# Kernel optimization log

Measured on AMD Instinct MI355X. Metric: run time of the kernel, lower is better.

## Reference

```python
import jax, jax.numpy as jnp
import numpy as np

B, T, S, L = 1, 2048, 512, 1024
C, H, Hk, D = 2048, 16, 4, 128
THETA = 10000.0


def setup_inputs() -> dict:
    key = jax.random.key(0)
    ks = jax.random.split(key, 9)
    sd = 0.02
    return {
        "x": jax.random.normal(ks[0], (B, T, C), jnp.float32),
        "stm": jax.random.normal(ks[1], (B, S, C), jnp.float32),
        "long_q": jax.random.normal(ks[2], (B, L, H, D), jnp.float32),
        "long_k": jax.random.normal(ks[3], (B, L, Hk, D), jnp.float32),
        "long_v": jax.random.normal(ks[4], (B, L, Hk, D), jnp.float32),
        "Wq": jax.random.normal(ks[5], (C, C), jnp.float32) * sd,
        "Wk": jax.random.normal(ks[6], (C, Hk * D), jnp.float32) * sd,
        "Wv": jax.random.normal(ks[7], (C, Hk * D), jnp.float32) * sd,
        "Wo": jax.random.normal(ks[8], (C, C), jnp.float32) * sd,
    }


def _rope_cos_sin(n, d, theta):
    # precompute_freqs_cis: freqs over even dims, angles t*freq
    freqs = 1.0 / (theta ** (jnp.arange(0, d, 2, dtype=jnp.float32) / d))
    ang = jnp.arange(n, dtype=jnp.float32)[:, None] * freqs[None, :]  # (n, d/2)
    return jnp.cos(ang), jnp.sin(ang)


def _apply_rope(x, cos, sin):
    # x: (B, n, h, D); complex-pair rotation over consecutive dims
    x1, x2 = x[..., 0::2], x[..., 1::2]
    c = cos[None, :, None, :]
    s = sin[None, :, None, :]
    r1 = x1 * c - x2 * s
    r2 = x1 * s + x2 * c
    return jnp.stack([r1, r2], axis=-1).reshape(x.shape)


def reference(x, stm, long_q, long_k, long_v, Wq, Wk, Wv, Wo):
    Bb, Tt, Cc = x.shape
    Ss, Ll = stm.shape[1], long_q.shape[1]
    seq = jnp.concatenate([stm, x], axis=1)  # (B, S+T, C)
    q = jnp.concatenate([long_q, (seq @ Wq).reshape(Bb, Ss + Tt, H, D)], axis=1)
    k = jnp.concatenate([long_k, (seq @ Wk).reshape(Bb, Ss + Tt, Hk, D)], axis=1)
    v = jnp.concatenate([long_v, (seq @ Wv).reshape(Bb, Ss + Tt, Hk, D)], axis=1)
    # inline RoPE on the last T+S positions only (memory bank keeps fixed encoding)
    cos, sin = _rope_cos_sin(Ss + Tt, D, THETA)
    q = q.at[:, Ll:].set(_apply_rope(q[:, Ll:], cos, sin))
    k = k.at[:, Ll:].set(_apply_rope(k[:, Ll:], cos, sin))
    tot = Ll + Ss + Tt
    # structured memory mask: causal over full stream, memory keys (< L+S) visible to all
    idx = jnp.arange(tot)
    mask = (idx[None, :] <= idx[:, None]) | (idx[None, :] < Ll + Ss)  # (tot, tot)
    # GQA: repeat_interleave kv heads
    rep = H // Hk
    kr = jnp.repeat(k, rep, axis=2)  # (B, tot, H, D)
    vr = jnp.repeat(v, rep, axis=2)
    att = jnp.einsum("bihd,bjhd->bhij", q, kr) * (1.0 / np.sqrt(D))
    att = jnp.where(mask[None, None], att, -jnp.inf)
    att = jax.nn.softmax(att, axis=-1)
    y = jnp.einsum("bhij,bjhd->bihd", att, vr).reshape(Bb, tot, Cc)
    y = y[:, -Tt:]  # keep only current-block outputs
    return y @ Wo
```

## Files before the change

### kernel.cpp

```cpp
#include <hip/hip_runtime.h>
#include <hip/hip_bf16.h>

typedef __attribute__((ext_vector_type(8))) short short8;
typedef __attribute__((ext_vector_type(4))) short short4v;
typedef __attribute__((ext_vector_type(4))) float f32x4;
typedef __attribute__((ext_vector_type(4))) float float4v;
typedef __attribute__((ext_vector_type(4))) int i32x4;

#define DEVFN static __device__ __forceinline__

#define T_N   2048
#define S_N   512
#define L_N   1024
#define C_N   2048
#define H_N   16
#define HK_N  4
#define D_N   128
#define ST_N  2560
#define TOT_N 3584
#define KV_N  512

DEVFN short f2bf(float f) {
  union { float f; unsigned u; } v; v.f = f;
  return (short)((v.u + 0x7FFFu + ((v.u >> 16) & 1u)) >> 16);
}
DEVFN float bf2f(short s) {
  union { unsigned u; float f; } v; v.u = ((unsigned)(unsigned short)s) << 16;
  return v.f;
}
DEVFN void gload16(const void* g, void* l) {
  __builtin_amdgcn_global_load_lds(
      (__attribute__((address_space(1))) void*)(g),
      (__attribute__((address_space(3))) void*)(l), 16, 0, 0);
}

#define Q_A (S_N * C_N / 4)
#define Q_B (Q_A + T_N * C_N / 4)
#define Q_C (Q_B + L_N * KV_N / 4)
#define Q_D (Q_C + L_N * KV_N / 4)
#define TAB_E (Q_D + ST_N * 64)
__global__ void k_setup(const float* __restrict__ x, const float* __restrict__ stm,
                        const float* __restrict__ lk, const float* __restrict__ lv,
                        short* __restrict__ seq, short* __restrict__ Kf,
                        short* __restrict__ Vf, float* __restrict__ ct,
                        float* __restrict__ st_) {
  int i = blockIdx.x * 256 + threadIdx.x;
  if (i < Q_D) {
    const float* src; short* dst; int off;
    if (i < Q_A)      { src = stm; dst = seq;                         off = i; }
    else if (i < Q_B) { src = x;   dst = seq + (size_t)S_N * C_N;     off = i - Q_A; }
    else if (i < Q_C) { src = lk;  dst = Kf;                          off = i - Q_B; }
    else              { src = lv;  dst = Vf;                          off = i - Q_C; }
    float4v v = reinterpret_cast<const float4v*>(src)[off];
    short4v o;
    o[0] = f2bf(v[0]); o[1] = f2bf(v[1]); o[2] = f2bf(v[2]); o[3] = f2bf(v[3]);
    reinterpret_cast<short4v*>(dst)[off] = o;
  } else {
    int j = i - Q_D;
    int p = j >> 6, fq = j & 63;
    float freq = expf(-(float)fq * (logf(10000.0f) / 64.0f));
    float ang = (float)p * freq;
    ct[j] = cosf(ang);
    st_[j] = sinf(ang);
  }
}

__global__ void k_tconv_all(const float* __restrict__ Wq, const float* __restrict__ Wk,
                            const float* __restrict__ Wv, const float* __restrict__ Wo,
                            short* __restrict__ WqT, short* __restrict__ WkT,
                            short* __restrict__ WvT, short* __restrict__ WoT) {
  __shared__ float tile[32][33];
  const int z = blockIdx.z;
  const float* in = (z == 0) ? Wq : (z == 1) ? Wk : (z == 2) ? Wv : Wo;
  short* outp     = (z == 0) ? WqT : (z == 1) ? WkT : (z == 2) ? WvT : WoT;
  const int cols = (z == 1 || z == 2) ? KV_N : C_N;
  if (blockIdx.x * 32 >= cols) return;
  int c0 = blockIdx.x * 32, r0 = blockIdx.y * 32;
  int tx = threadIdx.x, ty = threadIdx.y;
#pragma unroll
  for (int i = 0; i < 4; i++)
    tile[ty + i * 8][tx] = in[(size_t)(r0 + ty + i * 8) * cols + c0 + tx];
  __syncthreads();
#pragma unroll
  for (int i = 0; i < 4; i++)
    outp[(size_t)(c0 + ty + i * 8) * C_N + r0 + tx] = f2bf(tile[tx][ty + i * 8]);
}

__global__ void k_tv(const short* __restrict__ vf, short* __restrict__ vt) {
  __shared__ short tile[32][33];
  int hk = blockIdx.z;
  int r0 = blockIdx.x * 32;
  int d0 = blockIdx.y * 32;
  int tx = threadIdx.x, ty = threadIdx.y;
#pragma unroll
  for (int i = 0; i < 4; i++)
    tile[ty + i * 8][tx] = vf[(size_t)(r0 + ty + i * 8) * KV_N + hk * D_N + d0 + tx];
  __syncthreads();
  short* o = vt + (size_t)hk * D_N * TOT_N;
#pragma unroll
  for (int i = 0; i < 4; i++)
    o[(size_t)(d0 + ty + i * 8) * TOT_N + r0 + tx] = tile[tx][ty + i * 8];
}

template <bool OUT_F32>
__global__ __launch_bounds__(256) void k_gemm(
    const short* __restrict__ A, const short* __restrict__ Bt,
    void* __restrict__ C, int M, int N, int K) {
  __shared__ short lbuf[2 * 2 * 4096];
  const int tid = threadIdx.x;
  const int w = tid >> 6, l = tid & 63;
  const int l15 = l & 15, lh = l >> 4;
  const int rb = blockIdx.y << 7, cb = blockIdx.x << 7;
  const int wr = (w >> 1) << 6, wc = (w & 1) << 6;
  f32x4 acc[4][4] = {};
  const int c0 = tid, c1 = 256 + tid;
  const short* pa0 = &A[(size_t)(rb + (c0 >> 2)) * K + (((c0 ^ (c0 >> 2)) & 3) << 3)];
  const short* pa1 = &A[(size_t)(rb + (c1 >> 2)) * K + (((c1 ^ (c1 >> 2)) & 3) << 3)];
  const short* pb0 = &Bt[(size_t)(cb + (c0 >> 2)) * K + (((c0 ^ (c0 >> 2)) & 3) << 3)];
  const short* pb1 = &Bt[(size_t)(cb + (c1 >> 2)) * K + (((c1 ^ (c1 >> 2)) & 3) << 3)];
  const int offA0 = (w * 64) << 4, offA1 = ((256 + w * 64) << 4);
  char* lbase = (char*)lbuf;
  const int sw = (lh ^ (l15 & 3)) << 3;
  {
    gload16(pa0, lbase + offA0);
    gload16(pa1, lbase + offA1);
    gload16(pb0, lbase + 8192 + offA0);
    gload16(pb1, lbase + 8192 + offA1);
  }
  int cur = 0;
  for (int kt = 0; kt < K; kt += 32) {
    const bool more = (kt + 32 < K);
    if (more) {
      char* p = lbase + ((cur ^ 1) << 14);
      gload16(pa0 + kt + 32, p + offA0);
      gload16(pa1 + kt + 32, p + offA1);
      gload16(pb0 + kt + 32, p + 8192 + offA0);
      gload16(pb1 + kt + 32, p + 8192 + offA1);
      asm volatile("s_waitcnt vmcnt(4)" ::: "memory");
    } else {
      asm volatile("s_waitcnt vmcnt(0)" ::: "memory");
    }
    __builtin_amdgcn_s_barrier();
    __builtin_amdgcn_sched_barrier(0);
    const short* la = (const short*)(lbase + (cur << 14));
    const short* lb = (const short*)(lbase + (cur << 14) + 8192);
    short8 af[4], bg[4];
#pragma unroll
    for (int m = 0; m < 4; m++)
      af[m] = *reinterpret_cast<const short8*>(&la[(wr + m * 16 + l15) * 32 + sw]);
#pragma unroll
    for (int n = 0; n < 4; n++)
      bg[n] = *reinterpret_cast<const short8*>(&lb[(wc + n * 16 + l15) * 32 + sw]);
    __builtin_amdgcn_s_setprio(1);
#pragma unroll
    for (int m = 0; m < 4; m++)
#pragma unroll
      for (int n = 0; n < 4; n++)
        acc[m][n] = __builtin_amdgcn_mfma_f32_16x16x32_bf16(af[m], bg[n], acc[m][n], 0, 0, 0);
    __builtin_amdgcn_s_setprio(0);
    asm volatile("s_waitcnt lgkmcnt(0)" ::: "memory");
    __builtin_amdgcn_sched_barrier(0);
    __builtin_amdgcn_s_barrier();
    __builtin_amdgcn_sched_barrier(0);
    cur ^= 1;
  }
#pragma unroll
  for (int m = 0; m < 4; m++)
#pragma unroll
    for (int n = 0; n < 4; n++)
#pragma unroll
      for (int r = 0; r < 4; r++) {
        int row = rb + wr + m * 16 + lh * 4 + r;
        int col = cb + wc + n * 16 + l15;
        if (OUT_F32)
          reinterpret_cast<float*>(C)[(size_t)row * N + col] = acc[m][n][r];
        else
          reinterpret_cast<short*>(C)[(size_t)row * N + col] = f2bf(acc[m][n][r]);
      }
}

__global__ __launch_bounds__(256) void k_gemm_qkv(
    const short* __restrict__ A, const short* __restrict__ Bt,
    short* __restrict__ qbuf, short* __restrict__ Kf, short* __restrict__ Vf,
    const float* __restrict__ ct, const float* __restrict__ st_) {
  const int Kd = C_N;
  __shared__ short lbuf[2 * 2 * 4096];
  const int tid = threadIdx.x;
  const int w = tid >> 6, l = tid & 63;
  const int l15 = l & 15, lh = l >> 4;
  const int rb = blockIdx.y << 7, cb = blockIdx.x << 7;
  const int wr = (w >> 1) << 6, wc = (w & 1) << 6;
  f32x4 acc[4][4] = {};
  const int c0 = tid, c1 = 256 + tid;
  const short* pa0 = &A[(size_t)(rb + (c0 >> 2)) * Kd + (((c0 ^ (c0 >> 2)) & 3) << 3)];
  const short* pa1 = &A[(size_t)(rb + (c1 >> 2)) * Kd + (((c1 ^ (c1 >> 2)) & 3) << 3)];
  const short* pb0 = &Bt[(size_t)(cb + (c0 >> 2)) * Kd + (((c0 ^ (c0 >> 2)) & 3) << 3)];
  const short* pb1 = &Bt[(size_t)(cb + (c1 >> 2)) * Kd + (((c1 ^ (c1 >> 2)) & 3) << 3)];
  const int offA0 = (w * 64) << 4, offA1 = ((256 + w * 64) << 4);
  char* lbase = (char*)lbuf;
  const int sw = (lh ^ (l15 & 3)) << 3;
  {
    gload16(pa0, lbase + offA0);
    gload16(pa1, lbase + offA1);
    gload16(pb0, lbase + 8192 + offA0);
    gload16(pb1, lbase + 8192 + offA1);
  }
  int cur = 0;
  for (int kt = 0; kt < Kd; kt += 32) {
    const bool more = (kt + 32 < Kd);
    if (more) {
      char* p = lbase + ((cur ^ 1) << 14);
      gload16(pa0 + kt + 32, p + offA0);
      gload16(pa1 + kt + 32, p + offA1);
      gload16(pb0 + kt + 32, p + 8192 + offA0);
      gload16(pb1 + kt + 32, p + 8192 + offA1);
      asm volatile("s_waitcnt vmcnt(4)" ::: "memory");
    } else {
      asm volatile("s_waitcnt vmcnt(0)" ::: "memory");
    }
    __builtin_amdgcn_s_barrier();
    __builtin_amdgcn_sched_barrier(0);
    const short* la = (const short*)(lbase + (cur << 14));
    const short* lb = (const short*)(lbase + (cur << 14) + 8192);
    short8 af[4], bg[4];
#pragma unroll
    for (int m = 0; m < 4; m++)
      af[m] = *reinterpret_cast<const short8*>(&la[(wr + m * 16 + l15) * 32 + sw]);
#pragma unroll
    for (int n = 0; n < 4; n++)
      bg[n] = *reinterpret_cast<const short8*>(&lb[(wc + n * 16 + l15) * 32 + sw]);
    __builtin_amdgcn_s_setprio(1);
#pragma unroll
    for (int m = 0; m < 4; m++)
#pragma unroll
      for (int n = 0; n < 4; n++)
        acc[m][n] = __builtin_amdgcn_mfma_f32_16x16x32_bf16(af[m], bg[n], acc[m][n], 0, 0, 0);
    __builtin_amdgcn_s_setprio(0);
    asm volatile("s_waitcnt lgkmcnt(0)" ::: "memory");
    __builtin_amdgcn_sched_barrier(0);
    __builtin_amdgcn_s_barrier();
    __builtin_amdgcn_sched_barrier(0);
    cur ^= 1;
  }
#pragma unroll
  for (int m = 0; m < 4; m++)
#pragma unroll
    for (int n = 0; n < 4; n++) {
      int coln = cb + wc + n * 16 + l15;
      const bool do_rope = coln < 2560;
      const int fidx = (coln & 127) >> 1;
#pragma unroll
      for (int r = 0; r < 4; r++) {
        int row = rb + wr + m * 16 + lh * 4 + r;
        float v = acc[m][n][r];
        float other = __shfl_xor(v, 1, 64);
        if (do_rope) {
          float co = ct[row * 64 + fidx];
          float si = st_[row * 64 + fidx];
          v = (l15 & 1) ? (other * si + v * co) : (v * co - other * si);
        }
        short bv = f2bf(v);
        if (coln < 2048) {
          if (row >= 512) qbuf[(size_t)(row - 512) * C_N + coln] = bv;
        } else if (coln < 2560) {
          Kf[(size_t)(L_N + row) * KV_N + (coln - 2048)] = bv;
        } else {
          Vf[(size_t)(L_N + row) * KV_N + (coln - 2560)] = bv;
        }
      }
    }
}

__global__ __launch_bounds__(256) void k_attn(
    const short* __restrict__ Q,
    const short* __restrict__ Kf,
    const short* __restrict__ Vt,
    short* __restrict__ Y) {
  __shared__ short kl[2][64 * 128];
  __shared__ short vl[2][128 * 64];
  const int f = blockIdx.x;
  const int hk = f & 3;
  const int qraw = (f >> 2) & 31;
  const int hh = (f >> 7) & 3;
  const int qb = (f & 256) ? (31 - qraw) : qraw;
  const int h = hk * 4 + hh;
  const int tid = threadIdx.x, w = tid >> 6, l = tid & 63;
  const int l15 = l & 15, lh = l >> 4;
  const int qbase = qb << 6;
  const int qrow0 = qbase + (w << 4);
  short8 aq[4];
#pragma unroll
  for (int kb = 0; kb < 4; kb++)
    aq[kb] = *reinterpret_cast<const short8*>(
        &Q[(size_t)(qrow0 + l15) * C_N + h * D_N + kb * 32 + lh * 8]);
  short8 ones;
#pragma unroll
  for (int j = 0; j < 8; j++) ones[j] = (short)0x3F80;
  f32x4 yacc[8] = {};
  f32x4 lacc = {};
  float m_r = -3.0e38f;
  const float K2 = 0.12751744f;
  const float THR = 90.0f;
  const int nkt = (1663 + qbase) >> 6;
  const short* psk[4];
  const short* psv[4];
  int ldsoff[4];
#pragma unroll
  for (int it = 0; it < 4; it++) {
    int c = it * 256 + tid;
    int kr = c >> 4, kkc = c & 15;
    int pkr = (kr & 0x23) | ((kr & 0x0C) << 1) | ((kr >> 2) & 4);
    psk[it] = &Kf[(size_t)pkr * KV_N + hk * D_N + ((kkc ^ (kr & 7)) << 3)];
    int vrow = c >> 3, vkc = c & 7;
    psv[it] = &Vt[(size_t)hk * D_N * TOT_N + (size_t)vrow * TOT_N + ((vkc ^ (vrow & 7)) << 3)];
    ldsoff[it] = (it * 256 + w * 64) << 4;
  }
#pragma unroll
  for (int it = 0; it < 4; it++) gload16(psk[it], (char*)kl + ldsoff[it]);
#pragma unroll
  for (int it = 0; it < 4; it++) gload16(psv[it], (char*)vl + ldsoff[it]);
#pragma unroll
  for (int it = 0; it < 4; it++)
    gload16(psk[it] + 64 * KV_N, (char*)kl + 16384 + ldsoff[it]);
#pragma unroll
  for (int it = 0; it < 4; it++)
    gload16(psv[it] + 64, (char*)vl + 16384 + ldsoff[it]);
  for (int t = 0; t < nkt; t++) {
    if (t + 1 < nkt) asm volatile("s_waitcnt vmcnt(8)" ::: "memory");
    else             asm volatile("s_waitcnt vmcnt(0)" ::: "memory");
    __builtin_amdgcn_s_barrier();
    __builtin_amdgcn_sched_barrier(0);
    const char* kbuf = (const char*)kl + ((t & 1) << 14);
    const char* vbuf = (const char*)vl + ((t & 1) << 14);
    f32x4 s[4] = {};
    __builtin_amdgcn_s_setprio(1);
#pragma unroll
    for (int g = 0; g < 4; g++) {
      int row = g * 16 + l15;
#pragma unroll
      for (int kb = 0; kb < 4; kb++) {
        short8 bk = *reinterpret_cast<const short8*>(
            kbuf + row * 256 + ((((kb << 2) + lh) ^ (row & 7)) << 4));
        s[g] = __builtin_amdgcn_mfma_f32_16x16x32_bf16(bk, aq[kb], s[g], 0, 0, 0);
      }
    }
    __builtin_amdgcn_s_setprio(0);
    if ((t * 64 + 63) > (1536 + qrow0)) {
      int qi = qrow0 + l15;
#pragma unroll
      for (int g = 0; g < 4; g++)
#pragma unroll
        for (int r = 0; r < 4; r++) {
          int key = t * 64 + ((g >> 1) << 5) + (lh << 3) + ((g & 1) << 2) + r;
          if (key > 1536 + qi) s[g][r] = -3.0e38f;
        }
    }
    float lm = s[0][0];
#pragma unroll
    for (int g = 0; g < 4; g++)
#pragma unroll
      for (int r = 0; r < 4; r++) lm = fmaxf(lm, s[g][r]);
    if (!__all(lm <= m_r + THR)) {
      float rm = fmaxf(lm, __shfl_xor(lm, 16, 64));
      rm = fmaxf(rm, __shfl_xor(rm, 32, 64));
      float mn = fmaxf(m_r, rm);
      float scf = __builtin_amdgcn_exp2f((m_r - mn) * K2);
      m_r = mn;
#pragma unroll
      for (int r = 0; r < 4; r++) {
        float sc_c = __shfl(scf, lh * 4 + r, 64);
        lacc[r] *= sc_c;
#pragma unroll
        for (int dg = 0; dg < 8; dg++) yacc[dg][r] *= sc_c;
      }
    }
    const float mk = m_r * K2;
    float pv[16];
#pragma unroll
    for (int g = 0; g < 4; g++)
#pragma unroll
      for (int r = 0; r < 4; r++)
        pv[g * 4 + r] = __builtin_amdgcn_exp2f(s[g][r] * K2 - mk);
    union { i32x4 wv; short8 sv; } u0, u1;
#pragma unroll
    for (int j = 0; j < 4; j++) {
      unsigned w0, w1;
      int g0 = (j >> 1), b0 = g0 * 4 + 2 * (j & 1);
      int g1 = 2 + (j >> 1), b1 = g1 * 4 + 2 * (j & 1);
      asm("v_cvt_pk_bf16_f32 %0, %1, %2" : "=v"(w0) : "v"(pv[b0]), "v"(pv[b0 + 1]));
      asm("v_cvt_pk_bf16_f32 %0, %1, %2" : "=v"(w1) : "v"(pv[b1]), "v"(pv[b1 + 1]));
      u0.wv[j] = (int)w0;
      u1.wv[j] = (int)w1;
    }
    lacc = __builtin_amdgcn_mfma_f32_16x16x32_bf16(u0.sv, ones, lacc, 0, 0, 0);
    lacc = __builtin_amdgcn_mfma_f32_16x16x32_bf16(u1.sv, ones, lacc, 0, 0, 0);
    __builtin_amdgcn_s_setprio(1);
#pragma unroll
    for (int dg = 0; dg < 8; dg++) {
      int vrow = dg * 16 + l15;
      short8 bv0 = *reinterpret_cast<const short8*>(
          vbuf + (vrow << 7) + ((lh ^ (vrow & 7)) << 4));
      yacc[dg] = __builtin_amdgcn_mfma_f32_16x16x32_bf16(u0.sv, bv0, yacc[dg], 0, 0, 0);
      short8 bv1 = *reinterpret_cast<const short8*>(
          vbuf + (vrow << 7) + (((4 + lh) ^ (vrow & 7)) << 4));
      yacc[dg] = __builtin_amdgcn_mfma_f32_16x16x32_bf16(u1.sv, bv1, yacc[dg], 0, 0, 0);
    }
    __builtin_amdgcn_s_setprio(0);
    asm volatile("s_waitcnt lgkmcnt(0)" ::: "memory");
    __builtin_amdgcn_sched_barrier(0);
    __builtin_amdgcn_s_barrier();
    __builtin_amdgcn_sched_barrier(0);
    if (t + 2 < nkt) {
#pragma unroll
      for (int it = 0; it < 4; it++)
        gload16(psk[it] + (size_t)(t + 2) * 64 * KV_N, (char*)kl + ((t & 1) << 14) + ldsoff[it]);
#pragma unroll
      for (int it = 0; it < 4; it++)
        gload16(psv[it] + (size_t)(t + 2) * 64, (char*)vl + ((t & 1) << 14) + ldsoff[it]);
    }
  }
#pragma unroll
  for (int dg = 0; dg < 8; dg++)
#pragma unroll
    for (int r = 0; r < 4; r++) {
      int row = qrow0 + lh * 4 + r;
      int col = h * D_N + dg * 16 + l15;
      Y[(size_t)row * C_N + col] = f2bf(yacc[dg][r] / lacc[r]);
    }
}

extern "C" void kernel_launch(void* const* d_in, const int* in_sizes, int n_in,
                              void* d_out, int out_size, void* d_ws, size_t ws_size,
                              hipStream_t stream) {
  const float* x      = (const float*)d_in[0];
  const float* stm    = (const float*)d_in[1];
  const float* long_k = (const float*)d_in[3];
  const float* long_v = (const float*)d_in[4];
  const float* Wq     = (const float*)d_in[5];
  const float* Wk     = (const float*)d_in[6];
  const float* Wv     = (const float*)d_in[7];
  const float* Wo     = (const float*)d_in[8];
  float* out = (float*)d_out;

  short* seq  = (short*)d_ws;
  short* WqT  = seq  + (size_t)ST_N * C_N;
  short* WkT  = WqT  + (size_t)C_N * C_N;
  short* WvT  = WkT  + (size_t)KV_N * C_N;
  short* WoT  = WvT  + (size_t)KV_N * C_N;
  short* qbuf = WoT  + (size_t)C_N * C_N;
  short* Kf   = qbuf + (size_t)T_N * C_N;
  short* Vf   = Kf   + (size_t)TOT_N * KV_N;
  short* Vt   = Vf   + (size_t)TOT_N * KV_N;
  short* ybuf = Vt   + (size_t)TOT_N * KV_N;
  float* ctab = (float*)(ybuf + (size_t)T_N * C_N);
  float* stab = ctab + (size_t)ST_N * 64;

  k_setup<<<TAB_E / 256, 256, 0, stream>>>(x, stm, long_k, long_v, seq, Kf, Vf, ctab, stab);

  k_tconv_all<<<dim3(64, 64, 4), dim3(32, 8), 0, stream>>>(
      Wq, Wk, Wv, Wo, WqT, WkT, WvT, WoT);

  k_gemm_qkv<<<dim3(3072 / 128, ST_N / 128), 256, 0, stream>>>(
      seq, WqT, qbuf, Kf, Vf, ctab, stab);

  k_tv<<<dim3(TOT_N / 32, D_N / 32, HK_N), dim3(32, 8), 0, stream>>>(Vf, Vt);

  k_attn<<<512, 256, 0, stream>>>(qbuf, Kf, Vt, ybuf);

  k_gemm<true><<<dim3(C_N / 128, T_N / 128), 256, 0, stream>>>(ybuf, WoT, out, T_N, C_N, C_N);
}
```

Measured before the change: 193.8 us.

## Use 64x128 GEMM tiles with XCD-aware block remap and skip unused Q rows

Both the QKV and output-projection GEMMs move from 128x128 to 64x128 tiles on a 1D grid. The grid uses a remapped block index so neighbouring tiles land on the same XCD for better L2 sharing. The QKV GEMM no longer computes Q tiles for the short-term-memory rows, whose results were previously computed and then thrown away. Smaller tiles give more blocks and better balance across CUs, at the cost of less operand reuse per loaded tile and a shallower MFMA burst per barrier.

Result: no change. 195.8 us (+1.1%).

```diff
diff --git a/kernel.cpp b/kernel.cpp
--- a/kernel.cpp
+++ b/kernel.cpp
@@ -102,58 +102,57 @@
     o[(size_t)(d0 + ty + i * 8) * TOT_N + r0 + tx] = tile[tx][ty + i * 8];
 }
 
-template <bool OUT_F32>
-__global__ __launch_bounds__(256) void k_gemm(
+__global__ __launch_bounds__(256) void k_gemm_o(
     const short* __restrict__ A, const short* __restrict__ Bt,
-    void* __restrict__ C, int M, int N, int K) {
-  __shared__ short lbuf[2 * 2 * 4096];
+    float* __restrict__ C) {
+  __shared__ short lbuf[2 * 6144];
   const int tid = threadIdx.x;
   const int w = tid >> 6, l = tid & 63;
   const int l15 = l & 15, lh = l >> 4;
-  const int rb = blockIdx.y << 7, cb = blockIdx.x << 7;
-  const int wr = (w >> 1) << 6, wc = (w & 1) << 6;
-  f32x4 acc[4][4] = {};
-  const int c0 = tid, c1 = 256 + tid;
-  const short* pa0 = &A[(size_t)(rb + (c0 >> 2)) * K + (((c0 ^ (c0 >> 2)) & 3) << 3)];
-  const short* pa1 = &A[(size_t)(rb + (c1 >> 2)) * K + (((c1 ^ (c1 >> 2)) & 3) << 3)];
-  const short* pb0 = &Bt[(size_t)(cb + (c0 >> 2)) * K + (((c0 ^ (c0 >> 2)) & 3) << 3)];
-  const short* pb1 = &Bt[(size_t)(cb + (c1 >> 2)) * K + (((c1 ^ (c1 >> 2)) & 3) << 3)];
-  const int offA0 = (w * 64) << 4, offA1 = ((256 + w * 64) << 4);
+  const int f0 = blockIdx.x;
+  const int f = ((f0 & 7) << 6) + (f0 >> 3);
+  const int rb = (f >> 4) << 6, cb = (f & 15) << 7;
+  const int wr = (w >> 1) << 5, wc = (w & 1) << 6;
+  f32x4 acc[2][4] = {};
+  const int cA = tid;
+  const short* pa = &A[(size_t)(rb + (cA >> 2)) * 2048 + (((cA ^ (cA >> 2)) & 3) << 3)];
+  const int cB0 = tid, cB1 = 256 + tid;
+  const short* pb0 = &Bt[(size_t)(cb + (cB0 >> 2)) * 2048 + (((cB0 ^ (cB0 >> 2)) & 3) << 3)];
+  const short* pb1 = &Bt[(size_t)(cb + (cB1 >> 2)) * 2048 + (((cB1 ^ (cB1 >> 2)) & 3) << 3)];
+  const int offA  = (w * 64) << 4;
+  const int offB0 = 4096 + ((w * 64) << 4);
+  const int offB1 = 4096 + ((256 + w * 64) << 4);
   char* lbase = (char*)lbuf;
   const int sw = (lh ^ (l15 & 3)) << 3;
-  {
-    gload16(pa0, lbase + offA0);
-    gload16(pa1, lbase + offA1);
-    gload16(pb0, lbase + 8192 + offA0);
-    gload16(pb1, lbase + 8192 + offA1);
-  }
+  gload16(pa,  lbase + offA);
+  gload16(pb0, lbase + offB0);
+  gload16(pb1, lbase + offB1);
   int cur = 0;
-  for (int kt = 0; kt < K; kt += 32) {
-    const bool more = (kt + 32 < K);
+  for (int kt = 0; kt < 2048; kt += 32) {
+    const bool more = (kt + 32 < 2048);
     if (more) {
-      char* p = lbase + ((cur ^ 1) << 14);
-      gload16(pa0 + kt + 32, p + offA0);
-      gload16(pa1 + kt + 32, p + offA1);
-      gload16(pb0 + kt + 32, p + 8192 + offA0);
-      gload16(pb1 + kt + 32, p + 8192 + offA1);
-      asm volatile("s_waitcnt vmcnt(4)" ::: "memory");
+      char* p = lbase + (cur ^ 1) * 12288;
+      gload16(pa  + kt + 32, p + offA);
+      gload16(pb0 + kt + 32, p + offB0);
+      gload16(pb1 + kt + 32, p + offB1);
+      asm volatile("s_waitcnt vmcnt(3)" ::: "memory");
     } else {
       asm volatile("s_waitcnt vmcnt(0)" ::: "memory");
     }
     __builtin_amdgcn_s_barrier();
     __builtin_amdgcn_sched_barrier(0);
-    const short* la = (const short*)(lbase + (cur << 14));
-    const short* lb = (const short*)(lbase + (cur << 14) + 8192);
-    short8 af[4], bg[4];
-#pragma unroll
-    for (int m = 0; m < 4; m++)
+    const short* la = (const short*)(lbase + cur * 12288);
+    const short* lb = (const short*)(lbase + cur * 12288 + 4096);
+    short8 af[2], bg[4];
+#pragma unroll
+    for (int m = 0; m < 2; m++)
       af[m] = *reinterpret_cast<const short8*>(&la[(wr + m * 16 + l15) * 32 + sw]);
 #pragma unroll
     for (int n = 0; n < 4; n++)
       bg[n] = *reinterpret_cast<const short8*>(&lb[(wc + n * 16 + l15) * 32 + sw]);
     __builtin_amdgcn_s_setprio(1);
 #pragma unroll
-    for (int m = 0; m < 4; m++)
+    for (int m = 0; m < 2; m++)
 #pragma unroll
       for (int n = 0; n < 4; n++)
         acc[m][n] = __builtin_amdgcn_mfma_f32_16x16x32_bf16(af[m], bg[n], acc[m][n], 0, 0, 0);
@@ -165,17 +164,14 @@
     cur ^= 1;
   }
 #pragma unroll
-  for (int m = 0; m < 4; m++)
+  for (int m = 0; m < 2; m++)
 #pragma unroll
     for (int n = 0; n < 4; n++)
 #pragma unroll
       for (int r = 0; r < 4; r++) {
         int row = rb + wr + m * 16 + lh * 4 + r;
         int col = cb + wc + n * 16 + l15;
-        if (OUT_F32)
-          reinterpret_cast<float*>(C)[(size_t)row * N + col] = acc[m][n][r];
-        else
-          reinterpret_cast<short*>(C)[(size_t)row * N + col] = f2bf(acc[m][n][r]);
+        C[(size_t)row * 2048 + col] = acc[m][n][r];
       }
 }
 
@@ -183,55 +179,62 @@
     const short* __restrict__ A, const short* __restrict__ Bt,
     short* __restrict__ qbuf, short* __restrict__ Kf, short* __restrict__ Vf,
     const float* __restrict__ ct, const float* __restrict__ st_) {
-  const int Kd = C_N;
-  __shared__ short lbuf[2 * 2 * 4096];
+  __shared__ short lbuf[2 * 6144];
   const int tid = threadIdx.x;
   const int w = tid >> 6, l = tid & 63;
   const int l15 = l & 15, lh = l >> 4;
-  const int rb = blockIdx.y << 7, cb = blockIdx.x << 7;
-  const int wr = (w >> 1) << 6, wc = (w & 1) << 6;
-  f32x4 acc[4][4] = {};
-  const int c0 = tid, c1 = 256 + tid;
-  const short* pa0 = &A[(size_t)(rb + (c0 >> 2)) * Kd + (((c0 ^ (c0 >> 2)) & 3) << 3)];
-  const short* pa1 = &A[(size_t)(rb + (c1 >> 2)) * Kd + (((c1 ^ (c1 >> 2)) & 3) << 3)];
-  const short* pb0 = &Bt[(size_t)(cb + (c0 >> 2)) * Kd + (((c0 ^ (c0 >> 2)) & 3) << 3)];
-  const short* pb1 = &Bt[(size_t)(cb + (c1 >> 2)) * Kd + (((c1 ^ (c1 >> 2)) & 3) << 3)];
-  const int offA0 = (w * 64) << 4, offA1 = ((256 + w * 64) << 4);
+  const int f0 = blockIdx.x;
+  const int f = (f0 % 8) * 104 + f0 / 8;
+  int rb, cb;
+  if (f < 512) {
+    cb = (f & 15) << 7;
+    rb = 512 + ((f >> 4) << 6);
+  } else {
+    int g = f - 512;
+    cb = (16 + (g & 7)) << 7;
+    rb = (g >> 3) << 6;
+  }
+  const int wr = (w >> 1) << 5, wc = (w & 1) << 6;
+  f32x4 acc[2][4] = {};
+  const int cA = tid;
+  const short* pa = &A[(size_t)(rb + (cA >> 2)) * 2048 + (((cA ^ (cA >> 2)) & 3) << 3)];
+  const int cB0 = tid, cB1 = 256 + tid;
+  const short* pb0 = &Bt[(size_t)(cb + (cB0 >> 2)) * 2048 + (((cB0 ^ (cB0 >> 2)) & 3) << 3)];
+  const short* pb1 = &Bt[(size_t)(cb + (cB1 >> 2)) * 2048 + (((cB1 ^ (cB1 >> 2)) & 3) << 3)];
+  const int offA  = (w * 64) << 4;
+  const int offB0 = 4096 + ((w * 64) << 4);
+  const int offB1 = 4096 + ((256 + w * 64) << 4);
   char* lbase = (char*)lbuf;
   const int sw = (lh ^ (l15 & 3)) << 3;
-  {
-    gload16(pa0, lbase + offA0);
-    gload16(pa1, lbase + offA1);
-    gload16(pb0, lbase + 8192 + offA0);
-    gload16(pb1, lbase + 8192 + offA1);
-  }
+  gload16(pa,  lbase + offA);
+  gload16(pb0, lbase + offB0);
+  gload16(pb1, lbase + offB1);
   int cur = 0;
-  for (int kt = 0; kt < Kd; kt += 32) {
-    const bool more = (kt + 32 < Kd);
+  for (int kt = 0; kt < 2048; kt += 32) {
+    const bool more = (kt + 32 < 2048);
     if (more) {
-      char* p = lbase + ((cur ^ 1) << 14);
-      gload16(pa0 + kt + 32, p + offA0);
-      gload16(pa1 + kt + 32, p + offA1);
-      gload16(pb0 + kt + 32, p + 8192 + offA0);
-      gload16(pb1 + kt + 32, p + 8192 + offA1);
-      asm volatile("s_waitcnt vmcnt(4)" ::: "memory");
+      char* p = lbase + (cur ^ 1) * 12288;
+      gload16(pa  + kt + 32, p + offA);
+      gload16(pb0 + kt + 32, p + offB0);
+      gload16(pb1 + kt + 32, p + offB1);
+      asm volatile("s_waitcnt vmcnt(3)" ::: "memory");
     } else {
       asm volatile("s_waitcnt vmcnt(0)" ::: "memory");
     }
     __builtin_amdgcn_s_barrier();
     __builtin_amdgcn_sched_barrier(0);
-    const short* la = (const short*)(lbase + (cur << 14));
-    const short* lb = (const short*)(lbase + (cur << 14) + 8192);
-    short8 af[4], bg[4];
-#pragma unroll
-    for (int m = 0; m < 4; m++)
+    const short* la = (const short*)(lbase + cur * 12288);
+    const short* lb = (const short*)(lbase + cur * 12288 + 4096);
+    short8 af[2], bg[4];
+#pragma unroll
+    for (int m = 0; m < 2; m++)
       af[m] = *reinterpret_cast<const short8*>(&la[(wr + m * 16 + l15) * 32 + sw]);
 #pragma unroll
     for (int n = 0; n < 4; n++)
       bg[n] = *reinterpret_cast<const short8*>(&lb[(wc + n * 16 + l15) * 32 + sw]);
     __builtin_amdgcn_s_setprio(1);
 #pragma unroll
-    for (int m = 0; m < 4; m++)
+    for (int m = 0; m < 2; m++)
 #pragma unroll
       for (int n = 0; n < 4; n++)
         acc[m][n] = __builtin_amdgcn_mfma_f32_16x16x32_bf16(af[m], bg[n], acc[m][n], 0, 0, 0);
@@ -243,7 +246,7 @@
     cur ^= 1;
   }
 #pragma unroll
-  for (int m = 0; m < 4; m++)
+  for (int m = 0; m < 2; m++)
 #pragma unroll
     for (int n = 0; n < 4; n++) {
       int coln = cb + wc + n * 16 + l15;
@@ -460,12 +463,11 @@
   k_tconv_all<<<dim3(64, 64, 4), dim3(32, 8), 0, stream>>>(
       Wq, Wk, Wv, Wo, WqT, WkT, WvT, WoT);
 
-  k_gemm_qkv<<<dim3(3072 / 128, ST_N / 128), 256, 0, stream>>>(
-      seq, WqT, qbuf, Kf, Vf, ctab, stab);
+  k_gemm_qkv<<<832, 256, 0, stream>>>(seq, WqT, qbuf, Kf, Vf, ctab, stab);
 
   k_tv<<<dim3(TOT_N / 32, D_N / 32, HK_N), dim3(32, 8), 0, stream>>>(Vf, Vt);
 
   k_attn<<<512, 256, 0, stream>>>(qbuf, Kf, Vt, ybuf);
 
-  k_gemm<true><<<dim3(C_N / 128, T_N / 128), 256, 0, stream>>>(ybuf, WoT, out, T_N, C_N, C_N);
-}
+  k_gemm_o<<<512, 256, 0, stream>>>(ybuf, WoT, out);
+}
```
